# Kernel optimization log

Measured on AMD Instinct MI355X. Metric: run time of the kernel, lower is better.

Reference implementation:

```python
import jax, jax.numpy as jnp
import numpy as np

P = 4   # patch_size
H = 8   # num_heads


def setup_inputs() -> dict:
    key = jax.random.key(0)
    k0, k1, k2 = jax.random.split(key, 3)
    B, C, R = 8, 8, 64
    E = C * P ** 3  # 512
    s = 1.0 / np.sqrt(E)
    x = jax.random.normal(k0, (B, C, R, R, R), jnp.float32)
    in_proj_w = jax.random.normal(k1, (3 * E, E), jnp.float32) * s
    in_proj_b = jnp.zeros((3 * E,), jnp.float32)
    out_proj_w = jax.random.normal(k2, (E, E), jnp.float32) * s
    out_proj_b = jnp.zeros((E,), jnp.float32)
    return {"x": x, "in_proj_w": in_proj_w, "in_proj_b": in_proj_b,
            "out_proj_w": out_proj_w, "out_proj_b": out_proj_b}


def reference(x, in_proj_w, in_proj_b, out_proj_w, out_proj_b):
    B, C, Rx, Ry, Rz = x.shape
    p = P
    nx, ny, nz = Rx // p, Ry // p, Rz // p
    N = nx * ny * nz
    E = C * p ** 3
    dh = E // H

    # cyclic shift: move last patch to front == roll by +p on each spatial axis
    x = jnp.roll(x, (p, p, p), axis=(2, 3, 4))

    # window partition: (B,C,nx,p,ny,p,nz,p) -> (B, N, C*p^3), matching
    # unfold + flatten + permute + flatten of the torch code
    xw = (x.reshape(B, C, nx, p, ny, p, nz, p)
           .transpose(0, 2, 4, 6, 1, 3, 5, 7)
           .reshape(B, N, E))

    # nn.MultiheadAttention with batch_first=False: seq dim = B, batch dim = N
    qkv = jnp.einsum('bne,fe->bnf', xw, in_proj_w) + in_proj_b  # (B, N, 3E)
    q, k, v = jnp.split(qkv, 3, axis=-1)
    q = q.reshape(B, N, H, dh)
    k = k.reshape(B, N, H, dh)
    v = v.reshape(B, N, H, dh)
    scale = 1.0 / np.sqrt(dh)
    # attention over the B (sequence) axis, independently per window n and head h
    att = jax.nn.softmax(jnp.einsum('inhd,jnhd->nhij', q * scale, k), axis=-1)
    o = jnp.einsum('nhij,jnhd->inhd', att, v).reshape(B, N, E)
    o = jnp.einsum('bne,fe->bnf', o, out_proj_w) + out_proj_b  # (B, N, E)

    # torch reassembly via the cat-of-permute loops interleaves windows:
    # out[b, c, px*nx + ix, py*ny + iy, pz*nz + iz] = y[b, ix, iy, iz, c, px, py, pz]
    y = (o.reshape(B, nx, ny, nz, C, p, p, p)
          .transpose(0, 4, 5, 1, 6, 2, 7, 3)
          .reshape(B, C, Rx, Ry, Rz))

    # reverse cyclic shift: roll by -p on each spatial axis
    y = jnp.roll(y, (-p, -p, -p), axis=(2, 3, 4))
    return y
```

## Files before the change

### kernel.cpp

```cpp
#include <hip/hip_runtime.h>

typedef unsigned short u16;
typedef unsigned int u32;
typedef __bf16 bf16x8 __attribute__((ext_vector_type(8)));
typedef float f32x4 __attribute__((ext_vector_type(4)));
typedef unsigned short u16x8 __attribute__((ext_vector_type(8)));

__device__ __forceinline__ u16 f2bf(float f) {
  u32 u = __builtin_bit_cast(u32, f);
  u = (u + 0x7FFFu + ((u >> 16) & 1u)) >> 16;
  return (u16)u;
}
__device__ __forceinline__ float bf2f(u16 h) {
  u32 u = ((u32)h) << 16;
  return __builtin_bit_cast(float, u);
}

#define GLD16(gp, lp) __builtin_amdgcn_global_load_lds( \
    (const __attribute__((address_space(1))) u32*)(const void*)(gp), \
    (__attribute__((address_space(3))) u32*)(void*)(lp), 16, 0, 0)
#define SBAR() __builtin_amdgcn_s_barrier()
#define SCHED0() __builtin_amdgcn_sched_barrier(0)

__global__ __launch_bounds__(256) void cast_f32_bf16(const float* __restrict__ src,
                                                     u16* __restrict__ dst, int n4) {
  int i = blockIdx.x * 256 + threadIdx.x;
  if (i < n4) {
    float4 v = *(const float4*)(src + (size_t)i * 4);
    ushort4 u;
    u.x = f2bf(v.x); u.y = f2bf(v.y); u.z = f2bf(v.z); u.w = f2bf(v.w);
    *(ushort4*)(dst + (size_t)i * 4) = u;
  }
}

__global__ __launch_bounds__(256) void permute_in(const float* __restrict__ x,
                                                  u16* __restrict__ xw) {
  __shared__ float lds[128 * 64];
  int t = threadIdx.x;
  int bx = blockIdx.x;
  int b = blockIdx.y;
  int jx = bx >> 4, jy = bx & 15;
#pragma unroll
  for (int it = 0; it < 8; ++it) {
    int idx = t + it * 256;
    int row = idx >> 4, z4 = idx & 15;
    int c = row >> 4, qx = (row >> 2) & 3, qy = row & 3;
    int X = (jx * 4 + qx + 60) & 63;
    int Y = (jy * 4 + qy + 60) & 63;
    float4 v = *(const float4*)(x + ((((size_t)(b * 8 + c) * 64 + X) * 64 + Y) * 64 + z4 * 4));
    *(float4*)(lds + row * 64 + ((z4 ^ (row & 7)) << 2)) = v;
  }
  __syncthreads();
#pragma unroll
  for (int it = 0; it < 8; ++it) {
    int idx = t + it * 256;
    int jz = idx >> 7, r = idx & 127;
    int z4r = (jz + 15) & 15;
    float4 v = *(const float4*)(lds + r * 64 + ((z4r ^ (r & 7)) << 2));
    int nw = jx * 256 + jy * 16 + jz;
    ushort4 u;
    u.x = f2bf(v.x); u.y = f2bf(v.y); u.z = f2bf(v.z); u.w = f2bf(v.w);
    *(ushort4*)(xw + (size_t)(nw * 8 + b) * 512 + r * 4) = u;
  }
}

__global__ __launch_bounds__(512, 1) void gemm_qkv_attn(const u16* __restrict__ A,
                                                        const u16* __restrict__ W,
                                                        const float* __restrict__ bias,
                                                        u16* __restrict__ O) {
  __shared__ u16 smem[51200];
  u16* As = smem;
  u16* Bs = smem + 16384;

  int cpx = gridDim.x >> 3;
  int wg = (blockIdx.x & 7) * cpx + (blockIdx.x >> 3);
  int mb = wg >> 3, h = wg & 7;
  int m0 = mb * 256;

  int tid = threadIdx.x;
  int w = tid >> 6, l = tid & 63;
  int wr = w >> 2, wc = w & 3;
  int lr = l & 15, lg = l >> 4;

  int cA0 = w * 128 + l, cA1 = cA0 + 64;
  const u16* pA0 = A + (size_t)(m0 + (cA0 >> 2)) * 512 + (cA0 & 3) * 8;
  const u16* pA1 = A + (size_t)(m0 + (cA1 >> 2)) * 512 + (cA1 & 3) * 8;
  int cB0 = w * 96 + l;
  int cB1 = w * 96 + 64 + l;
  int br0 = cB0 >> 2, br1 = cB1 >> 2;
  const u16* pB0 = W + (size_t)((br0 >> 6) * 512 + h * 64 + (br0 & 63)) * 512 + (cB0 & 3) * 8;
  const u16* pB1 = W + (size_t)((br1 >> 6) * 512 + h * 64 + (br1 & 63)) * 512 + (cB1 & 3) * 8;

  f32x4 acc[8][3] = {};

#define STAGE_QKV(t) { int kadd = (t) * 32, d = (t) & 1;            \
    u16* ad = As + d * 8192 + w * 1024;                             \
    u16* bd = Bs + d * 6144 + w * 768;                              \
    GLD16(pA0 + kadd, ad);                                          \
    GLD16(pA1 + kadd, ad + 512);                                    \
    GLD16(pB0 + kadd, bd);                                          \
    if (l < 32) GLD16(pB1 + kadd, bd + 512); }

  STAGE_QKV(0);
  asm volatile("s_waitcnt vmcnt(0)" ::: "memory");
  SBAR(); SCHED0();

  for (int t = 0; t < 16; ++t) {
    if (t + 1 < 16) STAGE_QKV(t + 1);
    const u16* AsT = As + (t & 1) * 8192;
    const u16* BsT = Bs + (t & 1) * 6144;
    bf16x8 a[8], b[3];
#pragma unroll
    for (int m = 0; m < 8; ++m)
      a[m] = *(const bf16x8*)(AsT + (wr * 128 + m * 16 + lr) * 32 + lg * 8);
#pragma unroll
    for (int n = 0; n < 3; ++n)
      b[n] = *(const bf16x8*)(BsT + (wc * 48 + n * 16 + lr) * 32 + lg * 8);
#pragma unroll
    for (int m = 0; m < 8; ++m)
#pragma unroll
      for (int n = 0; n < 3; ++n)
        acc[m][n] = __builtin_amdgcn_mfma_f32_16x16x32_bf16(b[n], a[m], acc[m][n], 0, 0, 0);
    SCHED0();
    if (t + 1 < 16) asm volatile("s_waitcnt vmcnt(0)" ::: "memory");
    SBAR(); SCHED0();
  }

  u16* ct = smem;
#pragma unroll
  for (int n = 0; n < 3; ++n) {
    int col0 = wc * 48 + n * 16 + lg * 4;
    int gcol = ((col0 >> 6) << 9) + (h << 6) + (col0 & 63);
    float4 bv = *(const float4*)(bias + gcol);
#pragma unroll
    for (int m = 0; m < 8; ++m) {
      int row = wr * 128 + m * 16 + lr;
      ushort4 uu;
      uu.x = f2bf(acc[m][n][0] + bv.x);
      uu.y = f2bf(acc[m][n][1] + bv.y);
      uu.z = f2bf(acc[m][n][2] + bv.z);
      uu.w = f2bf(acc[m][n][3] + bv.w);
      *(ushort4*)(ct + row * 200 + col0) = uu;
    }
  }
  __syncthreads();

  int nw2 = tid >> 4, u4 = tid & 15, qi = u4 >> 1, jh = u4 & 1;
  const u16* qrow = ct + (nw2 * 8 + qi) * 200;
  float s4[4];
#pragma unroll
  for (int jj = 0; jj < 4; ++jj) {
    const u16* kr = ct + (nw2 * 8 + jh * 4 + jj) * 200 + 64;
    float sacc = 0.f;
#pragma unroll
    for (int dc = 0; dc < 8; ++dc) {
      u16x8 qv = *(const u16x8*)(qrow + dc * 8);
      u16x8 kv = *(const u16x8*)(kr + dc * 8);
#pragma unroll
      for (int e = 0; e < 8; ++e)
        sacc += bf2f((u16)qv[e]) * bf2f((u16)kv[e]);
    }
    s4[jj] = sacc * 0.125f;
  }
  float r0 = __shfl_xor(s4[0], 1), r1 = __shfl_xor(s4[1], 1);
  float r2 = __shfl_xor(s4[2], 1), r3 = __shfl_xor(s4[3], 1);
  float sm[8];
  if (jh == 0) {
    sm[0] = s4[0]; sm[1] = s4[1]; sm[2] = s4[2]; sm[3] = s4[3];
    sm[4] = r0; sm[5] = r1; sm[6] = r2; sm[7] = r3;
  } else {
    sm[0] = r0; sm[1] = r1; sm[2] = r2; sm[3] = r3;
    sm[4] = s4[0]; sm[5] = s4[1]; sm[6] = s4[2]; sm[7] = s4[3];
  }
  float mx = sm[0];
#pragma unroll
  for (int j = 1; j < 8; ++j) mx = fmaxf(mx, sm[j]);
  float p[8], psum = 0.f;
#pragma unroll
  for (int j = 0; j < 8; ++j) { p[j] = __expf(sm[j] - mx); psum += p[j]; }
  float inv = 1.f / psum;

  float ov[32];
#pragma unroll
  for (int e = 0; e < 32; ++e) ov[e] = 0.f;
#pragma unroll
  for (int j = 0; j < 8; ++j) {
    const u16* vr = ct + (nw2 * 8 + j) * 200 + 128 + jh * 32;
    float pj = p[j] * inv;
#pragma unroll
    for (int dc = 0; dc < 4; ++dc) {
      u16x8 vv = *(const u16x8*)(vr + dc * 8);
#pragma unroll
      for (int e = 0; e < 8; ++e)
        ov[dc * 8 + e] += pj * bf2f((u16)vv[e]);
    }
  }
  u32 pk[16];
#pragma unroll
  for (int e = 0; e < 16; ++e)
    pk[e] = (u32)f2bf(ov[2 * e]) | ((u32)f2bf(ov[2 * e + 1]) << 16);
  u32* dst = (u32*)(O + (size_t)(m0 + nw2 * 8 + qi) * 512 + h * 64 + jh * 32);
#pragma unroll
  for (int q4 = 0; q4 < 4; ++q4) {
    uint4 vq; vq.x = pk[q4 * 4]; vq.y = pk[q4 * 4 + 1];
    vq.z = pk[q4 * 4 + 2]; vq.w = pk[q4 * 4 + 3];
    *(uint4*)(dst + q4 * 4) = vq;
  }
}

__global__ __launch_bounds__(512, 1) void gemm_out(const u16* __restrict__ A,
                                                   const u16* __restrict__ W,
                                                   const float* __restrict__ bias,
                                                   u16* __restrict__ C) {
  __shared__ u16 smem[32768];
  u16* As = smem;
  u16* Bs = smem + 16384;

  int cpx = gridDim.x >> 3;
  int wg = (blockIdx.x & 7) * cpx + (blockIdx.x >> 3);
  int mb = wg >> 1, nb = wg & 1;
  int m0 = mb * 256, n0 = nb * 256;

  int tid = threadIdx.x;
  int w = tid >> 6, l = tid & 63;
  int wr = w >> 2, wc = w & 3;
  int lr = l & 15, lg = l >> 4;

  int cA0 = w * 128 + l, cA1 = cA0 + 64;
  const u16* pA0 = A + (size_t)(m0 + (cA0 >> 2)) * 512 + (cA0 & 3) * 8;
  const u16* pA1 = A + (size_t)(m0 + (cA1 >> 2)) * 512 + (cA1 & 3) * 8;
  const u16* pB0 = W + (size_t)(n0 + (cA0 >> 2)) * 512 + (cA0 & 3) * 8;
  const u16* pB1 = W + (size_t)(n0 + (cA1 >> 2)) * 512 + (cA1 & 3) * 8;

  f32x4 acc[8][4] = {};

#define STAGE_OUT(t) { int kadd = (t) * 32, d = (t) & 1;            \
    u16* ad = As + d * 8192 + w * 1024;                             \
    u16* bd = Bs + d * 8192 + w * 1024;                             \
    GLD16(pA0 + kadd, ad);                                          \
    GLD16(pA1 + kadd, ad + 512);                                    \
    GLD16(pB0 + kadd, bd);                                          \
    GLD16(pB1 + kadd, bd + 512); }

  STAGE_OUT(0);
  asm volatile("s_waitcnt vmcnt(0)" ::: "memory");
  SBAR(); SCHED0();

  for (int t = 0; t < 16; ++t) {
    if (t + 1 < 16) STAGE_OUT(t + 1);
    const u16* AsT = As + (t & 1) * 8192;
    const u16* BsT = Bs + (t & 1) * 8192;
    bf16x8 a[8], b[4];
#pragma unroll
    for (int m = 0; m < 8; ++m)
      a[m] = *(const bf16x8*)(AsT + (wr * 128 + m * 16 + lr) * 32 + lg * 8);
#pragma unroll
    for (int n = 0; n < 4; ++n)
      b[n] = *(const bf16x8*)(BsT + (wc * 64 + n * 16 + lr) * 32 + lg * 8);
#pragma unroll
    for (int m = 0; m < 8; ++m)
#pragma unroll
      for (int n = 0; n < 4; ++n)
        acc[m][n] = __builtin_amdgcn_mfma_f32_16x16x32_bf16(b[n], a[m], acc[m][n], 0, 0, 0);
    SCHED0();
    if (t + 1 < 16) asm volatile("s_waitcnt vmcnt(0)" ::: "memory");
    SBAR(); SCHED0();
  }

#pragma unroll
  for (int n = 0; n < 4; ++n) {
    int col0 = n0 + wc * 64 + n * 16 + lg * 4;
    float4 bv = *(const float4*)(bias + col0);
#pragma unroll
    for (int m = 0; m < 8; ++m) {
      size_t row = (size_t)(m0 + wr * 128 + m * 16 + lr);
      ushort4 uu;
      uu.x = f2bf(acc[m][n][0] + bv.x);
      uu.y = f2bf(acc[m][n][1] + bv.y);
      uu.z = f2bf(acc[m][n][2] + bv.z);
      uu.w = f2bf(acc[m][n][3] + bv.w);
      *(ushort4*)(C + row * 512 + col0) = uu;
    }
  }
}

__global__ __launch_bounds__(256) void permute_out(const u16* __restrict__ o2,
                                                   float* __restrict__ out) {
  __shared__ float lds[16 * 516];
  int t = threadIdx.x;
  int bx = blockIdx.x;
  int b = blockIdx.y;
  int ix = bx >> 4, iy = bx & 15;
  int n0 = ix * 256 + iy * 16;
#pragma unroll
  for (int it = 0; it < 8; ++it) {
    int idx = t + it * 256;
    int iz = idx >> 7, fq = idx & 127;
    ushort4 u = *(const ushort4*)(o2 + ((size_t)((n0 + iz) * 8 + b) * 512 + fq * 4));
    float4 v;
    v.x = bf2f(u.x); v.y = bf2f(u.y); v.z = bf2f(u.z); v.w = bf2f(u.w);
    *(float4*)(lds + iz * 516 + fq * 4) = v;
  }
  __syncthreads();
#pragma unroll
  for (int it = 0; it < 8; ++it) {
    int idx = t + it * 256;
    int fidx = idx >> 4, w4 = idx & 15;
    int c = fidx >> 4, px = (fidx >> 2) & 3, py = fidx & 3;
    int W0 = (w4 * 4 + 4) & 63;
    int pz = W0 >> 4, iz0 = W0 & 15;
    int fa = fidx * 4 + pz;
    float4 v;
    v.x = lds[(iz0 + 0) * 516 + fa];
    v.y = lds[(iz0 + 1) * 516 + fa];
    v.z = lds[(iz0 + 2) * 516 + fa];
    v.w = lds[(iz0 + 3) * 516 + fa];
    int uu = (px * 16 + ix + 60) & 63;
    int vv = (py * 16 + iy + 60) & 63;
    *(float4*)(out + ((((size_t)(b * 8 + c) * 64 + uu) * 64 + vv) * 64 + w4 * 4)) = v;
  }
}

extern "C" void kernel_launch(void* const* d_in, const int* in_sizes, int n_in,
                              void* d_out, int out_size, void* d_ws, size_t ws_size,
                              hipStream_t stream) {
  const float* x     = (const float*)d_in[0];
  const float* w_in  = (const float*)d_in[1];
  const float* b_in  = (const float*)d_in[2];
  const float* w_out = (const float*)d_in[3];
  const float* b_out = (const float*)d_in[4];
  float* out = (float*)d_out;

  char* ws = (char*)d_ws;
  u16* wq  = (u16*)(ws);
  u16* wo  = (u16*)(ws + 1572864);
  u16* xw2 = (u16*)(ws + 2097152);
  u16* o   = (u16*)(ws + 35651584);
  u16* o2  = (u16*)(ws + 69206016);

  cast_f32_bf16<<<768, 256, 0, stream>>>(w_in, wq, 196608);
  cast_f32_bf16<<<256, 256, 0, stream>>>(w_out, wo, 65536);
  permute_in<<<dim3(256, 8), 256, 0, stream>>>(x, xw2);
  gemm_qkv_attn<<<1024, 512, 0, stream>>>(xw2, wq, b_in, o);
  gemm_out<<<256, 512, 0, stream>>>(o, wo, b_out, o2);
  permute_out<<<dim3(256, 8), 256, 0, stream>>>(o2, out);
}
```

Baseline: 150.1 us.

## Deepen K tile to 64 with XOR-swizzled LDS and interleaved prefetch in GEMMs

```diff
diff --git a/kernel.cpp b/kernel.cpp
--- a/kernel.cpp
+++ b/kernel.cpp
@@ -68,9 +68,9 @@
                                                         const u16* __restrict__ W,
                                                         const float* __restrict__ bias,
                                                         u16* __restrict__ O) {
-  __shared__ u16 smem[51200];
+  __shared__ u16 smem[57344];
   u16* As = smem;
-  u16* Bs = smem + 16384;
+  u16* Bs = smem + 32768;
 
   int cpx = gridDim.x >> 3;
   int wg = (blockIdx.x & 7) * cpx + (blockIdx.x >> 3);
@@ -82,48 +82,80 @@
   int wr = w >> 2, wc = w & 3;
   int lr = l & 15, lg = l >> 4;
 
-  int cA0 = w * 128 + l, cA1 = cA0 + 64;
-  const u16* pA0 = A + (size_t)(m0 + (cA0 >> 2)) * 512 + (cA0 & 3) * 8;
-  const u16* pA1 = A + (size_t)(m0 + (cA1 >> 2)) * 512 + (cA1 & 3) * 8;
-  int cB0 = w * 96 + l;
-  int cB1 = w * 96 + 64 + l;
-  int br0 = cB0 >> 2, br1 = cB1 >> 2;
-  const u16* pB0 = W + (size_t)((br0 >> 6) * 512 + h * 64 + (br0 & 63)) * 512 + (cB0 & 3) * 8;
-  const u16* pB1 = W + (size_t)((br1 >> 6) * 512 + h * 64 + (br1 & 63)) * 512 + (cB1 & 3) * 8;
+  const u16* pa[4]; int dA[4];
+#pragma unroll
+  for (int i = 0; i < 4; ++i) {
+    int slot = w * 256 + i * 64 + l;
+    int row = slot >> 3, kg = (slot & 7) ^ (row & 7);
+    pa[i] = A + (size_t)(m0 + row) * 512 + kg * 8;
+    dA[i] = (w * 256 + i * 64) * 8;
+  }
+  const u16* pb[3]; int dB[3];
+#pragma unroll
+  for (int i = 0; i < 3; ++i) {
+    int slot = w * 192 + i * 64 + l;
+    int row = slot >> 3, kg = (slot & 7) ^ (row & 7);
+    int grow = (row >> 6) * 512 + h * 64 + (row & 63);
+    pb[i] = W + (size_t)grow * 512 + kg * 8;
+    dB[i] = (w * 192 + i * 64) * 8;
+  }
+
+  int cx0 = lg ^ (lr & 7), cx1 = cx0 ^ 4;
+  int aofs[2] = { (wr * 128 + lr) * 64 + cx0 * 8, (wr * 128 + lr) * 64 + cx1 * 8 };
+  int bofs[2] = { (wc * 48 + lr) * 64 + cx0 * 8, (wc * 48 + lr) * 64 + cx1 * 8 };
 
   f32x4 acc[8][3] = {};
 
-#define STAGE_QKV(t) { int kadd = (t) * 32, d = (t) & 1;            \
-    u16* ad = As + d * 8192 + w * 1024;                             \
-    u16* bd = Bs + d * 6144 + w * 768;                              \
-    GLD16(pA0 + kadd, ad);                                          \
-    GLD16(pA1 + kadd, ad + 512);                                    \
-    GLD16(pB0 + kadd, bd);                                          \
-    if (l < 32) GLD16(pB1 + kadd, bd + 512); }
-
-  STAGE_QKV(0);
+#pragma unroll
+  for (int i = 0; i < 4; ++i) GLD16(pa[i], As + dA[i]);
+#pragma unroll
+  for (int i = 0; i < 3; ++i) GLD16(pb[i], Bs + dB[i]);
   asm volatile("s_waitcnt vmcnt(0)" ::: "memory");
-  SBAR(); SCHED0();
-
-  for (int t = 0; t < 16; ++t) {
-    if (t + 1 < 16) STAGE_QKV(t + 1);
-    const u16* AsT = As + (t & 1) * 8192;
-    const u16* BsT = Bs + (t & 1) * 6144;
-    bf16x8 a[8], b[3];
-#pragma unroll
-    for (int m = 0; m < 8; ++m)
-      a[m] = *(const bf16x8*)(AsT + (wr * 128 + m * 16 + lr) * 32 + lg * 8);
-#pragma unroll
-    for (int n = 0; n < 3; ++n)
-      b[n] = *(const bf16x8*)(BsT + (wc * 48 + n * 16 + lr) * 32 + lg * 8);
-#pragma unroll
-    for (int m = 0; m < 8; ++m)
-#pragma unroll
-      for (int n = 0; n < 3; ++n)
-        acc[m][n] = __builtin_amdgcn_mfma_f32_16x16x32_bf16(b[n], a[m], acc[m][n], 0, 0, 0);
-    SCHED0();
-    if (t + 1 < 16) asm volatile("s_waitcnt vmcnt(0)" ::: "memory");
-    SBAR(); SCHED0();
+  SCHED0(); SBAR(); SCHED0();
+
+  for (int t = 0; t < 8; ++t) {
+    const u16* AsT = As + (t & 1) * 16384;
+    const u16* BsT = Bs + (t & 1) * 12288;
+    u16* Ad = As + ((t + 1) & 1) * 16384;
+    u16* Bd = Bs + ((t + 1) & 1) * 12288;
+    int nx = (t + 1) * 64;
+    bool st = (t < 7);
+    bf16x8 bfr[3][2];
+#pragma unroll
+    for (int pg = 0; pg < 4; ++pg) {
+      bf16x8 afr[2][2];
+#pragma unroll
+      for (int mi = 0; mi < 2; ++mi)
+#pragma unroll
+        for (int kk = 0; kk < 2; ++kk)
+          afr[mi][kk] = *(const bf16x8*)(AsT + aofs[kk] + (pg * 2 + mi) * 1024);
+      if (pg == 0) {
+#pragma unroll
+        for (int n = 0; n < 3; ++n)
+#pragma unroll
+          for (int kk = 0; kk < 2; ++kk)
+            bfr[n][kk] = *(const bf16x8*)(BsT + bofs[kk] + n * 1024);
+      }
+      if (pg == 0 && st) { GLD16(pa[0] + nx, Ad + dA[0]); GLD16(pa[1] + nx, Ad + dA[1]); }
+      if (pg == 1 && st) { GLD16(pa[2] + nx, Ad + dA[2]); GLD16(pa[3] + nx, Ad + dA[3]); }
+      if (pg == 2 && st) { GLD16(pb[0] + nx, Bd + dB[0]); GLD16(pb[1] + nx, Bd + dB[1]); }
+      if (pg == 3 && st) { GLD16(pb[2] + nx, Bd + dB[2]); }
+      SCHED0();
+      __builtin_amdgcn_s_setprio(1);
+#pragma unroll
+      for (int mi = 0; mi < 2; ++mi)
+#pragma unroll
+        for (int n = 0; n < 3; ++n)
+#pragma unroll
+          for (int kk = 0; kk < 2; ++kk)
+            acc[pg * 2 + mi][n] =
+                __builtin_amdgcn_mfma_f32_16x16x32_bf16(bfr[n][kk], afr[mi][kk],
+                                                        acc[pg * 2 + mi][n], 0, 0, 0);
+      __builtin_amdgcn_s_setprio(0);
+      SCHED0();
+    }
+    asm volatile("s_waitcnt vmcnt(0)" ::: "memory");
+    SCHED0(); SBAR(); SCHED0();
   }
 
   u16* ct = smem;
@@ -212,9 +244,9 @@
                                                    const u16* __restrict__ W,
                                                    const float* __restrict__ bias,
                                                    u16* __restrict__ C) {
-  __shared__ u16 smem[32768];
+  __shared__ u16 smem[65536];
   u16* As = smem;
-  u16* Bs = smem + 16384;
+  u16* Bs = smem + 32768;
 
   int cpx = gridDim.x >> 3;
   int wg = (blockIdx.x & 7) * cpx + (blockIdx.x >> 3);
@@ -226,45 +258,72 @@
   int wr = w >> 2, wc = w & 3;
   int lr = l & 15, lg = l >> 4;
 
-  int cA0 = w * 128 + l, cA1 = cA0 + 64;
-  const u16* pA0 = A + (size_t)(m0 + (cA0 >> 2)) * 512 + (cA0 & 3) * 8;
-  const u16* pA1 = A + (size_t)(m0 + (cA1 >> 2)) * 512 + (cA1 & 3) * 8;
-  const u16* pB0 = W + (size_t)(n0 + (cA0 >> 2)) * 512 + (cA0 & 3) * 8;
-  const u16* pB1 = W + (size_t)(n0 + (cA1 >> 2)) * 512 + (cA1 & 3) * 8;
+  const u16* pa[4]; const u16* pb[4]; int dS[4];
+#pragma unroll
+  for (int i = 0; i < 4; ++i) {
+    int slot = w * 256 + i * 64 + l;
+    int row = slot >> 3, kg = (slot & 7) ^ (row & 7);
+    pa[i] = A + (size_t)(m0 + row) * 512 + kg * 8;
+    pb[i] = W + (size_t)(n0 + row) * 512 + kg * 8;
+    dS[i] = (w * 256 + i * 64) * 8;
+  }
+
+  int cx0 = lg ^ (lr & 7), cx1 = cx0 ^ 4;
+  int aofs[2] = { (wr * 128 + lr) * 64 + cx0 * 8, (wr * 128 + lr) * 64 + cx1 * 8 };
+  int bofs[2] = { (wc * 64 + lr) * 64 + cx0 * 8, (wc * 64 + lr) * 64 + cx1 * 8 };
 
   f32x4 acc[8][4] = {};
 
-#define STAGE_OUT(t) { int kadd = (t) * 32, d = (t) & 1;            \
-    u16* ad = As + d * 8192 + w * 1024;                             \
-    u16* bd = Bs + d * 8192 + w * 1024;                             \
-    GLD16(pA0 + kadd, ad);                                          \
-    GLD16(pA1 + kadd, ad + 512);                                    \
-    GLD16(pB0 + kadd, bd);                                          \
-    GLD16(pB1 + kadd, bd + 512); }
-
-  STAGE_OUT(0);
+#pragma unroll
+  for (int i = 0; i < 4; ++i) GLD16(pa[i], As + dS[i]);
+#pragma unroll
+  for (int i = 0; i < 4; ++i) GLD16(pb[i], Bs + dS[i]);
   asm volatile("s_waitcnt vmcnt(0)" ::: "memory");
-  SBAR(); SCHED0();
-
-  for (int t = 0; t < 16; ++t) {
-    if (t + 1 < 16) STAGE_OUT(t + 1);
-    const u16* AsT = As + (t & 1) * 8192;
-    const u16* BsT = Bs + (t & 1) * 8192;
-    bf16x8 a[8], b[4];
-#pragma unroll
-    for (int m = 0; m < 8; ++m)
-      a[m] = *(const bf16x8*)(AsT + (wr * 128 + m * 16 + lr) * 32 + lg * 8);
-#pragma unroll
-    for (int n = 0; n < 4; ++n)
-      b[n] = *(const bf16x8*)(BsT + (wc * 64 + n * 16 + lr) * 32 + lg * 8);
-#pragma unroll
-    for (int m = 0; m < 8; ++m)
-#pragma unroll
-      for (int n = 0; n < 4; ++n)
-        acc[m][n] = __builtin_amdgcn_mfma_f32_16x16x32_bf16(b[n], a[m], acc[m][n], 0, 0, 0);
-    SCHED0();
-    if (t + 1 < 16) asm volatile("s_waitcnt vmcnt(0)" ::: "memory");
-    SBAR(); SCHED0();
+  SCHED0(); SBAR(); SCHED0();
+
+  for (int t = 0; t < 8; ++t) {
+    const u16* AsT = As + (t & 1) * 16384;
+    const u16* BsT = Bs + (t & 1) * 16384;
+    u16* Ad = As + ((t + 1) & 1) * 16384;
+    u16* Bd = Bs + ((t + 1) & 1) * 16384;
+    int nx = (t + 1) * 64;
+    bool st = (t < 7);
+    bf16x8 bfr[4][2];
+#pragma unroll
+    for (int pg = 0; pg < 4; ++pg) {
+      bf16x8 afr[2][2];
+#pragma unroll
+      for (int mi = 0; mi < 2; ++mi)
+#pragma unroll
+        for (int kk = 0; kk < 2; ++kk)
+          afr[mi][kk] = *(const bf16x8*)(AsT + aofs[kk] + (pg * 2 + mi) * 1024);
+      if (pg == 0) {
+#pragma unroll
+        for (int n = 0; n < 4; ++n)
+#pragma unroll
+          for (int kk = 0; kk < 2; ++kk)
+            bfr[n][kk] = *(const bf16x8*)(BsT + bofs[kk] + n * 1024);
+      }
+      if (pg == 0 && st) { GLD16(pa[0] + nx, Ad + dS[0]); GLD16(pa[1] + nx, Ad + dS[1]); }
+      if (pg == 1 && st) { GLD16(pa[2] + nx, Ad + dS[2]); GLD16(pa[3] + nx, Ad + dS[3]); }
+      if (pg == 2 && st) { GLD16(pb[0] + nx, Bd + dS[0]); GLD16(pb[1] + nx, Bd + dS[1]); }
+      if (pg == 3 && st) { GLD16(pb[2] + nx, Bd + dS[2]); GLD16(pb[3] + nx, Bd + dS[3]); }
+      SCHED0();
+      __builtin_amdgcn_s_setprio(1);
+#pragma unroll
+      for (int mi = 0; mi < 2; ++mi)
+#pragma unroll
+        for (int n = 0; n < 4; ++n)
+#pragma unroll
+          for (int kk = 0; kk < 2; ++kk)
+            acc[pg * 2 + mi][n] =
+                __builtin_amdgcn_mfma_f32_16x16x32_bf16(bfr[n][kk], afr[mi][kk],
+                                                        acc[pg * 2 + mi][n], 0, 0, 0);
+      __builtin_amdgcn_s_setprio(0);
+      SCHED0();
+    }
+    asm volatile("s_waitcnt vmcnt(0)" ::: "memory");
+    SCHED0(); SBAR(); SCHED0();
   }
 
 #pragma unroll
```

Measured after the change: 144.4 us. 1.04x faster.
